# Kernel tuning notes

Hardware: AMD Instinct MI355X
Metric: run time of the kernel (lower is better)

Reference implementation:

```python
import jax, jax.numpy as jnp
import numpy as np

NC, NM, E = 100000, 50000, 1000000
IN_C, IN_M, HID, OUT = 128, 64, 128, 64


def setup_inputs() -> dict:
    key = jax.random.key(0)
    ks = jax.random.split(key, 24)
    f = lambda k, shp: jax.random.normal(k, shp, dtype=jnp.float32) * 0.05
    inp = {
        'x_customer': f(ks[0], (NC, IN_C)),
        'x_merchant': f(ks[1], (NM, IN_M)),
        'W1cm_l': f(ks[2], (IN_C, HID)), 'W1cm_r': f(ks[3], (IN_M, HID)), 'b1_cm': f(ks[4], (HID,)),
        'W1mc_l': f(ks[5], (IN_M, HID)), 'W1mc_r': f(ks[6], (IN_C, HID)), 'b1_mc': f(ks[7], (HID,)),
        'W2cm_l': f(ks[8], (HID, HID)), 'W2cm_r': f(ks[9], (HID, HID)), 'b2_cm': f(ks[10], (HID,)),
        'W2mc_l': f(ks[11], (HID, HID)), 'W2mc_r': f(ks[12], (HID, HID)), 'b2_mc': f(ks[13], (HID,)),
        'Wout': f(ks[14], (HID, OUT)), 'bout': f(ks[15], (OUT,)),
        'ei_cm_src': jax.random.randint(ks[16], (E,), 0, NC, dtype=jnp.int32),
        'ei_cm_dst': jax.random.randint(ks[17], (E,), 0, NM, dtype=jnp.int32),
        'ei_mc_src': jax.random.randint(ks[18], (E,), 0, NM, dtype=jnp.int32),
        'ei_mc_dst': jax.random.randint(ks[19], (E,), 0, NC, dtype=jnp.int32),
    }
    return inp


def _sage(x_src, x_dst, src, dst, Wl, Wr, b, n_dst):
    # PyG SAGEConv: out = lin_l(mean_{j in N(i)} x_j) + lin_r(x_i)
    msg = x_src[src]                                        # [E, d_src] gather
    s = jax.ops.segment_sum(msg, dst, num_segments=n_dst)   # [n_dst, d_src]
    c = jax.ops.segment_sum(jnp.ones((src.shape[0],), x_src.dtype), dst, num_segments=n_dst)
    agg = s / jnp.maximum(c, 1.0)[:, None]                  # mean aggregation
    return agg @ Wl + b + x_dst @ Wr


def reference(x_customer, x_merchant,
              W1cm_l, W1cm_r, b1_cm, W1mc_l, W1mc_r, b1_mc,
              W2cm_l, W2cm_r, b2_cm, W2mc_l, W2mc_r, b2_mc,
              Wout, bout,
              ei_cm_src, ei_cm_dst, ei_mc_src, ei_mc_dst):
    # Layer 1 (bipartite): customer->merchant and merchant->customer; sum-merge is
    # trivial (one edge type per destination node type), then ReLU.
    h_m = jax.nn.relu(_sage(x_customer, x_merchant, ei_cm_src, ei_cm_dst, W1cm_l, W1cm_r, b1_cm, NM))
    h_c = jax.nn.relu(_sage(x_merchant, x_customer, ei_mc_src, ei_mc_dst, W1mc_l, W1mc_r, b1_mc, NC))
    # Layer 2 (hidden -> hidden)
    h_c2 = _sage(h_m, h_c, ei_mc_src, ei_mc_dst, W2mc_l, W2mc_r, b2_mc, NC)
    # Final linear on 'customer' embeddings
    return h_c2 @ Wout + bout
```

## Files before the change

### kernel.cpp

```cpp
#include <hip/hip_runtime.h>

#define NCUST 100000
#define NMERCH 50000
#define NEDGE 1000000
#define NTOT (NCUST + NMERCH)
#define HID 128
#define INC 128
#define INM 64
#define OUTD 64

#define SHIFT 9
#define BUCKW 512
#define NBUCKET ((NTOT + BUCKW - 1) / BUCKW)
#define EPB 4096
#define EPT (EPB / 256)

typedef __attribute__((ext_vector_type(8))) short s8v;
typedef __attribute__((ext_vector_type(4))) float f32x4;

__device__ __forceinline__ void splitpair(float a, float b, uint& hw, uint& lw) {
    uint ua = __float_as_uint(a), ub = __float_as_uint(b);
    uint ha = ua & 0xFFFF0000u, hb = ub & 0xFFFF0000u;
    hw = hb | (ua >> 16);
    float ra = a - __uint_as_float(ha);
    float rb = b - __uint_as_float(hb);
    lw = (__float_as_uint(rb) & 0xFFFF0000u) | (__float_as_uint(ra) >> 16);
}


__global__ __launch_bounds__(256) void hist_kernel(const int* __restrict__ cm_dst,
                                                   const int* __restrict__ mc_dst,
                                                   int* __restrict__ counts) {
    int idx = blockIdx.x * 256 + threadIdx.x;
    if (idx < NEDGE) {
        atomicAdd(&counts[cm_dst[idx]], 1);
    } else if (idx < 2 * NEDGE) {
        atomicAdd(&counts[NMERCH + mc_dst[idx - NEDGE]], 1);
    }
}

__global__ __launch_bounds__(256) void block_sums_kernel(const int* __restrict__ counts,
                                                         int* __restrict__ bsum) {
    int t = threadIdx.x;
    int idx = blockIdx.x * 1024 + t * 4;
    int4 v = make_int4(0, 0, 0, 0);
    if (idx + 3 < NTOT) {
        v = *(const int4*)(counts + idx);
    } else if (idx < NTOT) {
        v.x = counts[idx];
        if (idx + 1 < NTOT) v.y = counts[idx + 1];
        if (idx + 2 < NTOT) v.z = counts[idx + 2];
    }
    int s = v.x + v.y + v.z + v.w;
    __shared__ int sh[256];
    sh[t] = s;
    __syncthreads();
    for (int off = 128; off > 0; off >>= 1) {
        if (t < off) sh[t] += sh[t + off];
        __syncthreads();
    }
    if (t == 0) bsum[blockIdx.x] = sh[0];
}

__global__ __launch_bounds__(256) void scan_partials_kernel(const int* __restrict__ bsum,
                                                            int* __restrict__ bpre, int n) {
    int t = threadIdx.x;
    __shared__ int sh[256];
    int v = (t < n) ? bsum[t] : 0;
    sh[t] = v;
    __syncthreads();
    for (int off = 1; off < 256; off <<= 1) {
        int val = (t >= off) ? sh[t - off] : 0;
        __syncthreads();
        sh[t] += val;
        __syncthreads();
    }
    if (t < n) bpre[t] = sh[t] - v;
}

__global__ __launch_bounds__(256) void scan_chunks_kernel(const int* __restrict__ counts,
                                                          const int* __restrict__ bpre,
                                                          int* __restrict__ ro) {
    int t = threadIdx.x;
    int idx = blockIdx.x * 1024 + t * 4;
    int4 v = make_int4(0, 0, 0, 0);
    if (idx + 3 < NTOT) {
        v = *(const int4*)(counts + idx);
    } else if (idx < NTOT) {
        v.x = counts[idx];
        if (idx + 1 < NTOT) v.y = counts[idx + 1];
        if (idx + 2 < NTOT) v.z = counts[idx + 2];
    }
    int mysum = v.x + v.y + v.z + v.w;
    __shared__ int sh[256];
    sh[t] = mysum;
    __syncthreads();
    for (int off = 1; off < 256; off <<= 1) {
        int val = (t >= off) ? sh[t - off] : 0;
        __syncthreads();
        sh[t] += val;
        __syncthreads();
    }
    int base = bpre[blockIdx.x] + (sh[t] - mysum);
    int p0 = base;
    int p1 = p0 + v.x;
    int p2 = p1 + v.y;
    int p3 = p2 + v.z;
    if (idx < NTOT)     ro[idx]     = p0;
    if (idx + 1 < NTOT) ro[idx + 1] = p1;
    if (idx + 2 < NTOT) ro[idx + 2] = p2;
    if (idx + 3 < NTOT) ro[idx + 3] = p3;
    if (blockIdx.x == 0 && t == 0) ro[NTOT] = 2 * NEDGE;
}

__global__ __launch_bounds__(256) void init_bcur_kernel(const int* __restrict__ ro,
                                                        int* __restrict__ bucket_cursor) {
    int b = blockIdx.x * 256 + threadIdx.x;
    if (b < NBUCKET) bucket_cursor[b] = ro[b << SHIFT];
}

__global__ __launch_bounds__(256) void bin_kernel(const int* __restrict__ cm_src,
                                                  const int* __restrict__ cm_dst,
                                                  const int* __restrict__ mc_src,
                                                  const int* __restrict__ mc_dst,
                                                  int* __restrict__ bucket_cursor,
                                                  int2* __restrict__ pairs) {
    __shared__ int lhist[NBUCKET];
    __shared__ int lbase[NBUCKET];
    __shared__ int loff[NBUCKET];
    const int t = threadIdx.x;
    for (int i = t; i < NBUCKET; i += 256) { lhist[i] = 0; loff[i] = 0; }
    __syncthreads();
    const int base = blockIdx.x * EPB;
    int k_[EPT], s_[EPT];
#pragma unroll
    for (int i = 0; i < EPT; ++i) {
        int idx = base + t + i * 256;
        int key = -1, src = 0;
        if (idx < NEDGE) {
            key = cm_dst[idx];
            src = cm_src[idx];
        } else if (idx < 2 * NEDGE) {
            key = NMERCH + mc_dst[idx - NEDGE];
            src = mc_src[idx - NEDGE];
        }
        k_[i] = key;
        s_[i] = src;
        if (key >= 0) atomicAdd(&lhist[key >> SHIFT], 1);
    }
    __syncthreads();
    for (int b = t; b < NBUCKET; b += 256) {
        int c = lhist[b];
        if (c > 0) lbase[b] = atomicAdd(&bucket_cursor[b], c);
    }
    __syncthreads();
#pragma unroll
    for (int i = 0; i < EPT; ++i) {
        if (k_[i] >= 0) {
            int bk = k_[i] >> SHIFT;
            int p = lbase[bk] + atomicAdd(&loff[bk], 1);
            pairs[p] = make_int2(k_[i], s_[i]);
        }
    }
}

__global__ __launch_bounds__(256) void fillb_kernel(const int2* __restrict__ pairs,
                                                    const int* __restrict__ ro,
                                                    int* __restrict__ csr) {
    __shared__ int cur[BUCKW];
    const int b = blockIdx.x, t = threadIdx.x;
    const int kb = b << SHIFT;
    const int ke = (kb + BUCKW < NTOT) ? kb + BUCKW : NTOT;
    for (int i = t; i < ke - kb; i += 256) cur[i] = ro[kb + i];
    __syncthreads();
    const int start = ro[kb];
    const int end = ro[ke];
    for (int i = start + t; i < end; i += 256) {
        int2 rec = pairs[i];
        int p = atomicAdd(&cur[rec.x - kb], 1);
        csr[p] = rec.y;
    }
}


__global__ __launch_bounds__(256) void agg_cm_kernel(const float* __restrict__ xc,
                                                     const int* __restrict__ csr,
                                                     const int* __restrict__ ro,
                                                     float* __restrict__ aggm) {
    int node = blockIdx.x * 4 + (threadIdx.x >> 6);
    int lane = threadIdx.x & 63;
    if (node >= NMERCH) return;
    int start = ro[node], end = ro[node + 1];
    float2 a0 = {0.f, 0.f}, a1 = {0.f, 0.f}, a2 = {0.f, 0.f}, a3 = {0.f, 0.f};
    int e = start;
    for (; e + 4 <= end; e += 4) {
        int s0 = csr[e], s1 = csr[e + 1], s2 = csr[e + 2], s3 = csr[e + 3];
        float2 v0 = *(const float2*)(xc + (size_t)s0 * INC + lane * 2);
        float2 v1 = *(const float2*)(xc + (size_t)s1 * INC + lane * 2);
        float2 v2 = *(const float2*)(xc + (size_t)s2 * INC + lane * 2);
        float2 v3 = *(const float2*)(xc + (size_t)s3 * INC + lane * 2);
        a0.x += v0.x; a0.y += v0.y;
        a1.x += v1.x; a1.y += v1.y;
        a2.x += v2.x; a2.y += v2.y;
        a3.x += v3.x; a3.y += v3.y;
    }
    for (; e < end; ++e) {
        int s0 = csr[e];
        float2 v0 = *(const float2*)(xc + (size_t)s0 * INC + lane * 2);
        a0.x += v0.x; a0.y += v0.y;
    }
    int deg = end - start;
    float cnt = (float)(deg > 0 ? deg : 1);
    float2 o;
    o.x = (a0.x + a1.x + a2.x + a3.x) / cnt;
    o.y = (a0.y + a1.y + a2.y + a3.y) / cnt;
    *(float2*)(aggm + (size_t)node * HID + lane * 2) = o;
}

__global__ __launch_bounds__(256) void agg_mc_kernel(const float* __restrict__ xm,
                                                     const float* __restrict__ t2p,
                                                     const int* __restrict__ csr,
                                                     const int* __restrict__ ro,
                                                     float* __restrict__ agg_c,
                                                     float* __restrict__ aggT2) {
    int node = blockIdx.x * 4 + (threadIdx.x >> 6);
    int lane = threadIdx.x & 63;
    if (node >= NCUST) return;
    int start = ro[NMERCH + node], end = ro[NMERCH + node + 1];
    float a0 = 0.f, a1 = 0.f, a2 = 0.f, a3 = 0.f;
    float h0 = 0.f, h1 = 0.f, h2 = 0.f, h3 = 0.f;
    int e = start;
    for (; e + 4 <= end; e += 4) {
        int s0 = csr[e], s1 = csr[e + 1], s2 = csr[e + 2], s3 = csr[e + 3];
        a0 += xm[(size_t)s0 * INM + lane];
        a1 += xm[(size_t)s1 * INM + lane];
        a2 += xm[(size_t)s2 * INM + lane];
        a3 += xm[(size_t)s3 * INM + lane];
        h0 += t2p[(size_t)s0 * OUTD + lane];
        h1 += t2p[(size_t)s1 * OUTD + lane];
        h2 += t2p[(size_t)s2 * OUTD + lane];
        h3 += t2p[(size_t)s3 * OUTD + lane];
    }
    for (; e < end; ++e) {
        int s0 = csr[e];
        a0 += xm[(size_t)s0 * INM + lane];
        h0 += t2p[(size_t)s0 * OUTD + lane];
    }
    int deg = end - start;
    float cnt = (float)(deg > 0 ? deg : 1);
    agg_c[(size_t)node * INM + lane] = (a0 + a1 + a2 + a3) / cnt;
    aggT2[(size_t)node * OUTD + lane] = (h0 + h1 + h2 + h3) / cnt;
}


__global__ __launch_bounds__(64) void small_mm_kernel(const float* __restrict__ Wa,
                                                      const float* __restrict__ Wb,
                                                      float* __restrict__ o) {
    __shared__ float row[128];
    int r = blockIdx.x, j = threadIdx.x;
    for (int k = j; k < 128; k += 64) row[k] = Wa[r * 128 + k];
    __syncthreads();
    float acc = 0.f;
    for (int k = 0; k < 128; ++k) acc = fmaf(row[k], Wb[k * 64 + j], acc);
    o[r * 64 + j] = acc;
}

__global__ void bprime_kernel(const float* __restrict__ b2, const float* __restrict__ Wout,
                              const float* __restrict__ bout, float* __restrict__ bprime) {
    int j = threadIdx.x;
    float acc = bout[j];
    for (int k = 0; k < HID; ++k) acc = fmaf(b2[k], Wout[k * OUTD + j], acc);
    bprime[j] = acc;
}


__global__ __launch_bounds__(256) void wprep_kernel(const float* __restrict__ w0,
                                                    const float* __restrict__ w1,
                                                    const float* __restrict__ w2,
                                                    const float* __restrict__ w3,
                                                    const float* __restrict__ w4,
                                                    const float* __restrict__ w5,
                                                    short* __restrict__ planes) {
    int b = blockIdx.x;
    const float* src;
    int N, kt, hoff, loff;
    if (b < 4)       { src = w0; N = 128; kt = b;      hoff = 0;      loff = 16384; }
    else if (b < 6)  { src = w1; N = 128; kt = b - 4;  hoff = 32768;  loff = 40960; }
    else if (b < 8)  { src = w2; N = 128; kt = b - 6;  hoff = 49152;  loff = 57344; }
    else if (b < 12) { src = w3; N = 128; kt = b - 8;  hoff = 65536;  loff = 81920; }
    else if (b < 16) { src = w4; N = 64;  kt = b - 12; hoff = 98304;  loff = 106496; }
    else             { src = w5; N = 64;  kt = b - 16; hoff = 114688; loff = 122880; }

    for (int slot = threadIdx.x; slot < N * 4; slot += 256) {
        int n = slot % N, kg = slot / N;
        uint hw[4], lw[4];
#pragma unroll
        for (int p = 0; p < 4; ++p) {
            float a = src[(kt * 32 + kg * 8 + 2 * p) * N + n];
            float c = src[(kt * 32 + kg * 8 + 2 * p + 1) * N + n];
            splitpair(a, c, hw[p], lw[p]);
        }
        size_t eoff = (size_t)((kt * 4 + kg) * N + n) * 8;
        *(int4*)&planes[hoff + eoff] = make_int4(hw[0], hw[1], hw[2], hw[3]);
        *(int4*)&planes[loff + eoff] = make_int4(lw[0], lw[1], lw[2], lw[3]);
    }
}


template <int KA, int KB, int NOUT, bool RELU, bool HASBIAS, bool HASADD>
__global__ __launch_bounds__(256) void mfma_gemm(const float* __restrict__ A,
                                                 const float* __restrict__ B,
                                                 const short* __restrict__ WAh,
                                                 const short* __restrict__ WAl,
                                                 const short* __restrict__ WBh,
                                                 const short* __restrict__ WBl,
                                                 const float* __restrict__ bias,
                                                 const float* __restrict__ add,
                                                 float* __restrict__ out, int M) {
    constexpr int NSA = KA / 32, NSB = KB / 32, NS = NSA + NSB;
    constexpr int CBN = NOUT / 32;

    __shared__ int4 AhL[2][512];
    __shared__ int4 AlL[2][512];

    const int t = threadIdx.x;
    const int lane = t & 63;
    const int wv = t >> 6;
    const int wr = wv >> 1;
    const int wc = wv & 1;
    const int rowbase = blockIdx.x * 128;
    const int srow = t >> 1, kh = t & 1;

    float4 pa[4];

    auto gload = [&](int s) {
        const float* src;
        int lda, ks;
        if (s < NSA) { src = A; lda = KA; ks = s * 32; }
        else         { src = B; lda = KB; ks = (s - NSA) * 32; }
        const int grow = rowbase + srow;
        if (grow < M) {
            const float* p = src + (size_t)grow * lda + ks + kh * 16;
            pa[0] = *(const float4*)(p);
            pa[1] = *(const float4*)(p + 4);
            pa[2] = *(const float4*)(p + 8);
            pa[3] = *(const float4*)(p + 12);
        } else {
            pa[0] = pa[1] = pa[2] = pa[3] = make_float4(0.f, 0.f, 0.f, 0.f);
        }
    };

    auto stage = [&](int bb) {
        uint h[8], l[8];
        splitpair(pa[0].x, pa[0].y, h[0], l[0]);
        splitpair(pa[0].z, pa[0].w, h[1], l[1]);
        splitpair(pa[1].x, pa[1].y, h[2], l[2]);
        splitpair(pa[1].z, pa[1].w, h[3], l[3]);
        splitpair(pa[2].x, pa[2].y, h[4], l[4]);
        splitpair(pa[2].z, pa[2].w, h[5], l[5]);
        splitpair(pa[3].x, pa[3].y, h[6], l[6]);
        splitpair(pa[3].z, pa[3].w, h[7], l[7]);
        const int base0 = (2 * kh) * 128 + srow;
        const int base1 = base0 + 128;
        AhL[bb][base0] = make_int4(h[0], h[1], h[2], h[3]);
        AhL[bb][base1] = make_int4(h[4], h[5], h[6], h[7]);
        AlL[bb][base0] = make_int4(l[0], l[1], l[2], l[3]);
        AlL[bb][base1] = make_int4(l[4], l[5], l[6], l[7]);
    };

    f32x4 acc[4][CBN];
#pragma unroll
    for (int rb = 0; rb < 4; ++rb)
#pragma unroll
        for (int cb = 0; cb < CBN; ++cb) acc[rb][cb] = (f32x4){0.f, 0.f, 0.f, 0.f};

    const int kgl = lane >> 4, ln = lane & 15;

    gload(0);
    stage(0);
    for (int s = 0; s < NS; ++s) {
        if (s + 1 < NS) gload(s + 1);
        __syncthreads();
        const short *wph_, *wpl_;
        int wb;
        if (s < NSA) { wph_ = WAh; wpl_ = WAl; wb = s; }
        else         { wph_ = WBh; wpl_ = WBl; wb = s - NSA; }
        const s8v* wph = (const s8v*)wph_;
        const s8v* wpl = (const s8v*)wpl_;
        s8v bh[CBN], bl[CBN];
#pragma unroll
        for (int cb = 0; cb < CBN; ++cb) {
            int n = wc * (NOUT / 2) + cb * 16 + ln;
            int idx = (wb * 4 + kgl) * NOUT + n;
            bh[cb] = wph[idx];
            bl[cb] = wpl[idx];
        }
        const int bb = s & 1;
#pragma unroll
        for (int rb = 0; rb < 4; ++rb) {
            int row = wr * 64 + rb * 16 + ln;
            s8v ah = *(const s8v*)&AhL[bb][kgl * 128 + row];
            s8v al = *(const s8v*)&AlL[bb][kgl * 128 + row];
#pragma unroll
            for (int cb = 0; cb < CBN; ++cb) {
                acc[rb][cb] = __builtin_amdgcn_mfma_f32_16x16x32_bf16(ah, bh[cb], acc[rb][cb], 0, 0, 0);
                acc[rb][cb] = __builtin_amdgcn_mfma_f32_16x16x32_bf16(ah, bl[cb], acc[rb][cb], 0, 0, 0);
                acc[rb][cb] = __builtin_amdgcn_mfma_f32_16x16x32_bf16(al, bh[cb], acc[rb][cb], 0, 0, 0);
            }
        }
        if (s + 1 < NS) stage((s + 1) & 1);
    }

#pragma unroll
    for (int cb = 0; cb < CBN; ++cb) {
        int col = wc * (NOUT / 2) + cb * 16 + ln;
        float bv = HASBIAS ? bias[col] : 0.f;
#pragma unroll
        for (int rb = 0; rb < 4; ++rb) {
#pragma unroll
            for (int i = 0; i < 4; ++i) {
                int grow = rowbase + wr * 64 + rb * 16 + kgl * 4 + i;
                if (grow < M) {
                    float o = acc[rb][cb][i] + bv;
                    if (HASADD) o += add[(size_t)grow * NOUT + col];
                    if (RELU) o = fmaxf(o, 0.f);
                    out[(size_t)grow * NOUT + col] = o;
                }
            }
        }
    }
}


extern "C" void kernel_launch(void* const* d_in, const int* in_sizes, int n_in,
                              void* d_out, int out_size, void* d_ws, size_t ws_size,
                              hipStream_t stream) {
    const float* x_c    = (const float*)d_in[0];
    const float* x_m    = (const float*)d_in[1];
    const float* W1cm_l = (const float*)d_in[2];
    const float* W1cm_r = (const float*)d_in[3];
    const float* b1_cm  = (const float*)d_in[4];
    const float* W1mc_l = (const float*)d_in[5];
    const float* W1mc_r = (const float*)d_in[6];
    const float* b1_mc  = (const float*)d_in[7];
    const float* W2mc_l = (const float*)d_in[11];
    const float* W2mc_r = (const float*)d_in[12];
    const float* b2_mc  = (const float*)d_in[13];
    const float* Wout   = (const float*)d_in[14];
    const float* bout   = (const float*)d_in[15];
    const int* cm_src   = (const int*)d_in[16];
    const int* cm_dst   = (const int*)d_in[17];
    const int* mc_src   = (const int*)d_in[18];
    const int* mc_dst   = (const int*)d_in[19];
    float* out = (float*)d_out;

    char* ws = (char*)d_ws;
    size_t off = 0;
    auto bump = [&](size_t bytes) -> char* {
        off = (off + 255) & ~(size_t)255;
        char* p = ws + off;
        off += bytes;
        return p;
    };
    int* counts   = (int*)bump((size_t)NTOT * 4);
    int* ro       = (int*)bump((size_t)(NTOT + 1) * 4);
    int* bcur     = (int*)bump((size_t)NBUCKET * 4);
    int* bsum     = (int*)bump(256 * 4);
    int* bpre     = (int*)bump(256 * 4);
    int* csr      = (int*)bump((size_t)2 * NEDGE * 4);
    float* bufA   = (float*)bump((size_t)NCUST * HID * 4);
    float* t2p    = (float*)bump((size_t)NMERCH * OUTD * 4);
    float* agg_c  = (float*)bump((size_t)NCUST * INM * 4);
    float* aggT2  = (float*)bump((size_t)NCUST * OUTD * 4);
    float* h_c    = (float*)bump((size_t)NCUST * HID * 4);
    float* w2ro   = (float*)bump((size_t)HID * OUTD * 4);
    float* w2lo   = (float*)bump((size_t)HID * OUTD * 4);
    float* bpr    = (float*)bump((size_t)OUTD * 4);
    short* planes = (short*)bump((size_t)131072 * 2);

    float* t_agg_m = bufA;
    float* h_m     = bufA + (size_t)NMERCH * HID;
    int2* pairs    = (int2*)h_c;

    const int NBLK = (NTOT + 1023) / 1024;

    small_mm_kernel<<<128, 64, 0, stream>>>(W2mc_r, Wout, w2ro);
    small_mm_kernel<<<128, 64, 0, stream>>>(W2mc_l, Wout, w2lo);
    bprime_kernel<<<1, 64, 0, stream>>>(b2_mc, Wout, bout, bpr);
    wprep_kernel<<<20, 256, 0, stream>>>(W1cm_l, W1cm_r, W1mc_l, W1mc_r, w2ro, w2lo, planes);

    hipMemsetAsync(counts, 0, (size_t)NTOT * 4, stream);
    hist_kernel<<<(2 * NEDGE + 255) / 256, 256, 0, stream>>>(cm_dst, mc_dst, counts);
    block_sums_kernel<<<NBLK, 256, 0, stream>>>(counts, bsum);
    scan_partials_kernel<<<1, 256, 0, stream>>>(bsum, bpre, NBLK);
    scan_chunks_kernel<<<NBLK, 256, 0, stream>>>(counts, bpre, ro);
    init_bcur_kernel<<<(NBUCKET + 255) / 256, 256, 0, stream>>>(ro, bcur);
    bin_kernel<<<(2 * NEDGE + EPB - 1) / EPB, 256, 0, stream>>>(cm_src, cm_dst, mc_src, mc_dst,
                                                                bcur, pairs);
    fillb_kernel<<<NBUCKET, 256, 0, stream>>>(pairs, ro, csr);

    short* Pcml_h = planes;           short* Pcml_l = planes + 16384;
    short* Pcmr_h = planes + 32768;   short* Pcmr_l = planes + 40960;
    short* Pmcl_h = planes + 49152;   short* Pmcl_l = planes + 57344;
    short* Pmcr_h = planes + 65536;   short* Pmcr_l = planes + 81920;
    short* Pro_h  = planes + 98304;   short* Pro_l  = planes + 106496;
    short* Plo_h  = planes + 114688;  short* Plo_l  = planes + 122880;

    agg_cm_kernel<<<NMERCH / 4, 256, 0, stream>>>(x_c, csr, ro, t_agg_m);
    mfma_gemm<128, 64, 128, true, true, false><<<(NMERCH + 127) / 128, 256, 0, stream>>>(
        t_agg_m, x_m, Pcml_h, Pcml_l, Pcmr_h, Pcmr_l, b1_cm, nullptr, h_m, NMERCH);

    mfma_gemm<128, 0, 64, false, false, false><<<(NMERCH + 127) / 128, 256, 0, stream>>>(
        h_m, nullptr, Plo_h, Plo_l, nullptr, nullptr, nullptr, nullptr, t2p, NMERCH);

    agg_mc_kernel<<<NCUST / 4, 256, 0, stream>>>(x_m, t2p, csr, ro, agg_c, aggT2);

    mfma_gemm<64, 128, 128, true, true, false><<<(NCUST + 127) / 128, 256, 0, stream>>>(
        agg_c, x_c, Pmcl_h, Pmcl_l, Pmcr_h, Pmcr_l, b1_mc, nullptr, h_c, NCUST);

    mfma_gemm<128, 0, 64, false, true, true><<<(NCUST + 127) / 128, 256, 0, stream>>>(
        h_c, nullptr, Pro_h, Pro_l, nullptr, nullptr, bpr, aggT2, out, NCUST);
}
```

Measured before the change: 529.6 us.

## Build CSR via bucket-level counting and per-bucket local scan instead of global histogram

Replaces the per-node global atomic histogram plus the three-kernel prefix scan with a per-bucket histogram built in shared memory, a single-block scan over the roughly 293 buckets, and a per-bucket node histogram and scan inside the fill kernel, which now also writes the row offsets. This removes 2M global atomics on node counters, a 600KB memset and several small launches. In exchange the fill kernel reads the bucket's pairs twice and runs a 512-wide shared-memory scan per bucket.

```diff
diff --git a/kernel.cpp b/kernel.cpp
--- a/kernel.cpp
+++ b/kernel.cpp
@@ -28,102 +28,61 @@
 }
 
 
-__global__ __launch_bounds__(256) void hist_kernel(const int* __restrict__ cm_dst,
-                                                   const int* __restrict__ mc_dst,
-                                                   int* __restrict__ counts) {
-    int idx = blockIdx.x * 256 + threadIdx.x;
-    if (idx < NEDGE) {
-        atomicAdd(&counts[cm_dst[idx]], 1);
-    } else if (idx < 2 * NEDGE) {
-        atomicAdd(&counts[NMERCH + mc_dst[idx - NEDGE]], 1);
-    }
-}
-
-__global__ __launch_bounds__(256) void block_sums_kernel(const int* __restrict__ counts,
-                                                         int* __restrict__ bsum) {
-    int t = threadIdx.x;
-    int idx = blockIdx.x * 1024 + t * 4;
-    int4 v = make_int4(0, 0, 0, 0);
-    if (idx + 3 < NTOT) {
-        v = *(const int4*)(counts + idx);
-    } else if (idx < NTOT) {
-        v.x = counts[idx];
-        if (idx + 1 < NTOT) v.y = counts[idx + 1];
-        if (idx + 2 < NTOT) v.z = counts[idx + 2];
-    }
-    int s = v.x + v.y + v.z + v.w;
-    __shared__ int sh[256];
-    sh[t] = s;
-    __syncthreads();
-    for (int off = 128; off > 0; off >>= 1) {
-        if (t < off) sh[t] += sh[t + off];
+__global__ __launch_bounds__(256) void bcount_kernel(const int* __restrict__ cm_dst,
+                                                     const int* __restrict__ mc_dst,
+                                                     int* __restrict__ bcnt) {
+    __shared__ int lh[NBUCKET];
+    const int t = threadIdx.x;
+    for (int i = t; i < NBUCKET; i += 256) lh[i] = 0;
+    __syncthreads();
+    const int base = blockIdx.x * EPB;
+#pragma unroll
+    for (int i = 0; i < EPT; ++i) {
+        int idx = base + t + i * 256;
+        if (idx < NEDGE) {
+            atomicAdd(&lh[cm_dst[idx] >> SHIFT], 1);
+        } else if (idx < 2 * NEDGE) {
+            atomicAdd(&lh[(NMERCH + mc_dst[idx - NEDGE]) >> SHIFT], 1);
+        }
+    }
+    __syncthreads();
+    for (int i = t; i < NBUCKET; i += 256) {
+        int c = lh[i];
+        if (c > 0) atomicAdd(&bcnt[i], c);
+    }
+}
+
+__global__ __launch_bounds__(512) void scan_buckets_kernel(const int* __restrict__ bcnt,
+                                                           int* __restrict__ bbase,
+                                                           int* __restrict__ bcur,
+                                                           int* __restrict__ ro) {
+    __shared__ int sh[512];
+    const int t = threadIdx.x;
+    int v = (t < NBUCKET) ? bcnt[t] : 0;
+    sh[t] = v;
+    __syncthreads();
+    for (int off = 1; off < 512; off <<= 1) {
+        int x = (t >= off) ? sh[t - off] : 0;
         __syncthreads();
-    }
-    if (t == 0) bsum[blockIdx.x] = sh[0];
-}
-
-__global__ __launch_bounds__(256) void scan_partials_kernel(const int* __restrict__ bsum,
-                                                            int* __restrict__ bpre, int n) {
-    int t = threadIdx.x;
-    __shared__ int sh[256];
-    int v = (t < n) ? bsum[t] : 0;
-    sh[t] = v;
-    __syncthreads();
-    for (int off = 1; off < 256; off <<= 1) {
-        int val = (t >= off) ? sh[t - off] : 0;
+        sh[t] += x;
         __syncthreads();
-        sh[t] += val;
-        __syncthreads();
-    }
-    if (t < n) bpre[t] = sh[t] - v;
-}
-
-__global__ __launch_bounds__(256) void scan_chunks_kernel(const int* __restrict__ counts,
-                                                          const int* __restrict__ bpre,
-                                                          int* __restrict__ ro) {
-    int t = threadIdx.x;
-    int idx = blockIdx.x * 1024 + t * 4;
-    int4 v = make_int4(0, 0, 0, 0);
-    if (idx + 3 < NTOT) {
-        v = *(const int4*)(counts + idx);
-    } else if (idx < NTOT) {
-        v.x = counts[idx];
-        if (idx + 1 < NTOT) v.y = counts[idx + 1];
-        if (idx + 2 < NTOT) v.z = counts[idx + 2];
-    }
-    int mysum = v.x + v.y + v.z + v.w;
-    __shared__ int sh[256];
-    sh[t] = mysum;
-    __syncthreads();
-    for (int off = 1; off < 256; off <<= 1) {
-        int val = (t >= off) ? sh[t - off] : 0;
-        __syncthreads();
-        sh[t] += val;
-        __syncthreads();
-    }
-    int base = bpre[blockIdx.x] + (sh[t] - mysum);
-    int p0 = base;
-    int p1 = p0 + v.x;
-    int p2 = p1 + v.y;
-    int p3 = p2 + v.z;
-    if (idx < NTOT)     ro[idx]     = p0;
-    if (idx + 1 < NTOT) ro[idx + 1] = p1;
-    if (idx + 2 < NTOT) ro[idx + 2] = p2;
-    if (idx + 3 < NTOT) ro[idx + 3] = p3;
-    if (blockIdx.x == 0 && t == 0) ro[NTOT] = 2 * NEDGE;
-}
-
-__global__ __launch_bounds__(256) void init_bcur_kernel(const int* __restrict__ ro,
-                                                        int* __restrict__ bucket_cursor) {
-    int b = blockIdx.x * 256 + threadIdx.x;
-    if (b < NBUCKET) bucket_cursor[b] = ro[b << SHIFT];
+    }
+    if (t < NBUCKET) {
+        int e = sh[t] - v;
+        bbase[t] = e;
+        bcur[t] = e;
+    }
+    if (t == 0) {
+        bbase[NBUCKET] = 2 * NEDGE;
+        ro[NTOT] = 2 * NEDGE;
+    }
 }
 
 __global__ __launch_bounds__(256) void bin_kernel(const int* __restrict__ cm_src,
                                                   const int* __restrict__ cm_dst,
                                                   const int* __restrict__ mc_src,
                                                   const int* __restrict__ mc_dst,
-                                                  int* __restrict__ bucket_cursor,
+                                                  int* __restrict__ bcur,
                                                   int2* __restrict__ pairs) {
     __shared__ int lhist[NBUCKET];
     __shared__ int lbase[NBUCKET];
@@ -151,7 +110,7 @@
     __syncthreads();
     for (int b = t; b < NBUCKET; b += 256) {
         int c = lhist[b];
-        if (c > 0) lbase[b] = atomicAdd(&bucket_cursor[b], c);
+        if (c > 0) lbase[b] = atomicAdd(&bcur[b], c);
     }
     __syncthreads();
 #pragma unroll
@@ -164,18 +123,34 @@
     }
 }
 
-__global__ __launch_bounds__(256) void fillb_kernel(const int2* __restrict__ pairs,
-                                                    const int* __restrict__ ro,
+__global__ __launch_bounds__(512) void fillb_kernel(const int2* __restrict__ pairs,
+                                                    const int* __restrict__ bbase,
+                                                    int* __restrict__ ro,
                                                     int* __restrict__ csr) {
+    __shared__ int hist[BUCKW];
     __shared__ int cur[BUCKW];
     const int b = blockIdx.x, t = threadIdx.x;
     const int kb = b << SHIFT;
-    const int ke = (kb + BUCKW < NTOT) ? kb + BUCKW : NTOT;
-    for (int i = t; i < ke - kb; i += 256) cur[i] = ro[kb + i];
-    __syncthreads();
-    const int start = ro[kb];
-    const int end = ro[ke];
-    for (int i = start + t; i < end; i += 256) {
+    const int nk = (kb + BUCKW < NTOT) ? BUCKW : (NTOT - kb);
+    hist[t] = 0;
+    __syncthreads();
+    const int start = bbase[b], end = bbase[b + 1];
+    for (int i = start + t; i < end; i += 512) atomicAdd(&hist[pairs[i].x - kb], 1);
+    __syncthreads();
+    int v = hist[t];
+    cur[t] = v;
+    __syncthreads();
+    for (int off = 1; off < 512; off <<= 1) {
+        int x = (t >= off) ? cur[t - off] : 0;
+        __syncthreads();
+        cur[t] += x;
+        __syncthreads();
+    }
+    int pos = start + cur[t] - v;
+    if (t < nk) ro[kb + t] = pos;
+    cur[t] = pos;
+    __syncthreads();
+    for (int i = start + t; i < end; i += 512) {
         int2 rec = pairs[i];
         int p = atomicAdd(&cur[rec.x - kb], 1);
         csr[p] = rec.y;
@@ -462,11 +437,10 @@
         off += bytes;
         return p;
     };
-    int* counts   = (int*)bump((size_t)NTOT * 4);
     int* ro       = (int*)bump((size_t)(NTOT + 1) * 4);
+    int* bcnt     = (int*)bump((size_t)NBUCKET * 4);
+    int* bbase    = (int*)bump((size_t)(NBUCKET + 1) * 4);
     int* bcur     = (int*)bump((size_t)NBUCKET * 4);
-    int* bsum     = (int*)bump(256 * 4);
-    int* bpre     = (int*)bump(256 * 4);
     int* csr      = (int*)bump((size_t)2 * NEDGE * 4);
     float* bufA   = (float*)bump((size_t)NCUST * HID * 4);
     float* t2p    = (float*)bump((size_t)NMERCH * OUTD * 4);
@@ -482,22 +456,17 @@
     float* h_m     = bufA + (size_t)NMERCH * HID;
     int2* pairs    = (int2*)h_c;
 
-    const int NBLK = (NTOT + 1023) / 1024;
-
     small_mm_kernel<<<128, 64, 0, stream>>>(W2mc_r, Wout, w2ro);
     small_mm_kernel<<<128, 64, 0, stream>>>(W2mc_l, Wout, w2lo);
     bprime_kernel<<<1, 64, 0, stream>>>(b2_mc, Wout, bout, bpr);
     wprep_kernel<<<20, 256, 0, stream>>>(W1cm_l, W1cm_r, W1mc_l, W1mc_r, w2ro, w2lo, planes);
 
-    hipMemsetAsync(counts, 0, (size_t)NTOT * 4, stream);
-    hist_kernel<<<(2 * NEDGE + 255) / 256, 256, 0, stream>>>(cm_dst, mc_dst, counts);
-    block_sums_kernel<<<NBLK, 256, 0, stream>>>(counts, bsum);
-    scan_partials_kernel<<<1, 256, 0, stream>>>(bsum, bpre, NBLK);
-    scan_chunks_kernel<<<NBLK, 256, 0, stream>>>(counts, bpre, ro);
-    init_bcur_kernel<<<(NBUCKET + 255) / 256, 256, 0, stream>>>(ro, bcur);
+    hipMemsetAsync(bcnt, 0, (size_t)NBUCKET * 4, stream);
+    bcount_kernel<<<(2 * NEDGE + EPB - 1) / EPB, 256, 0, stream>>>(cm_dst, mc_dst, bcnt);
+    scan_buckets_kernel<<<1, 512, 0, stream>>>(bcnt, bbase, bcur, ro);
     bin_kernel<<<(2 * NEDGE + EPB - 1) / EPB, 256, 0, stream>>>(cm_src, cm_dst, mc_src, mc_dst,
                                                                 bcur, pairs);
-    fillb_kernel<<<NBUCKET, 256, 0, stream>>>(pairs, ro, csr);
+    fillb_kernel<<<NBUCKET, 512, 0, stream>>>(pairs, bbase, ro, csr);
 
     short* Pcml_h = planes;           short* Pcml_l = planes + 16384;
     short* Pcmr_h = planes + 32768;   short* Pcmr_l = planes + 40960;
```

Measured after the change: 462.1 us. 12.8% less time.
